# Kernel tuning notes

Hardware: AMD Instinct MI355X
Metric: run time of the kernel (lower is better)

## Reference

```python
import jax, jax.numpy as jnp
import numpy as np
from jax import lax

N = 2_097_152  # grid length
WENO5_MULT_BIAS = 0.1


def _conv1d(x, w, b, pad):
    # x: [1, C_in, L], w: [C_out, C_in, K] -> [1, C_out, L]
    y = lax.conv_general_dilated(x, w, window_strides=(1,), padding=[(pad, pad)],
                                 dimension_numbers=('NCH', 'OIH', 'NCH'))
    return y + b[None, :, None]


def _inner_nn_weno5(dif, w1, b1, w2, b2, w3, b3, w4, b4, w5, b5, w6, b6):
    # dif: [N] -> multiplier signal [N] in (0,1) via sigmoid
    x = dif[None, None, :]
    x = jax.nn.elu(_conv1d(x, w1, b1, 2))
    x = jax.nn.elu(_conv1d(x, w2, b2, 2))
    x = jax.nn.elu(_conv1d(x, w3, b3, 0))
    x = jax.nn.elu(_conv1d(x, w4, b4, 0))
    x = jax.nn.elu(_conv1d(x, w5, b5, 1))
    x = jax.nn.sigmoid(_conv1d(x, w6, b6, 0))
    return x[0, 0, :]


def _avg_diff(uu):
    # centered average of forward differences, replicated at the edges -> [N]
    dif = uu[1:] - uu[:-1]
    dif_left = jnp.concatenate([dif, dif[-1:]])
    dif_right = jnp.concatenate([dif[:1], dif])
    return 0.5 * dif_left + 0.5 * dif_right


def _fluxes_minus(u):
    f0 = (11 * u[3:-2] - 7 * u[4:-1] + 2 * u[5:]) / 6
    f1 = (2 * u[2:-3] + 5 * u[3:-2] - u[4:-1]) / 6
    f2 = (-u[1:-4] + 5 * u[2:-3] + 2 * u[3:-2]) / 6
    return f0, f1, f2


def _betas_minus(u):
    b0 = 13 / 12 * (u[3:-2] - 2 * u[4:-1] + u[5:]) ** 2 + 1 / 4 * (3 * u[3:-2] - 4 * u[4:-1] + u[5:]) ** 2
    b1 = 13 / 12 * (u[2:-3] - 2 * u[3:-2] + u[4:-1]) ** 2 + 1 / 4 * (u[2:-3] - u[4:-1]) ** 2
    b2 = 13 / 12 * (u[1:-4] - 2 * u[2:-3] + u[3:-2]) ** 2 + 1 / 4 * (u[1:-4] - 4 * u[2:-3] + 3 * u[3:-2]) ** 2
    return b0, b1, b2


def _weno5(uu, e, beta_mult):
    # w5_minus=True, mweno=True, mapped=False, trainable=True branch
    ur = uu[1:]
    ul = uu[:-1]
    fp = _fluxes_minus(ur)
    fn = _fluxes_minus(ul)
    bp = _betas_minus(ur)
    bn = _betas_minus(ul)
    # multipliers bm[3+shift:-3+shift] for shift in {-1,0,1}
    mul = (beta_mult[2:-4], beta_mult[3:-3], beta_mult[4:-2])
    bp = [b * m for b, m in zip(bp, mul)]
    bn = [b * m for b, m in zip(bn, mul)]
    ds = (1 / 10, 6 / 10, 3 / 10)

    def omegas_mweno(bs):
        brs = (bs[2] - bs[0]) ** 2
        o = [d / (e + b) ** 2 * (brs + (e + b) ** 2) for b, d in zip(bs, ds)]
        s = o[0] + o[1] + o[2]
        return [x / s for x in o]

    op = omegas_mweno(bp)
    on = omegas_mweno(bn)
    fluxp = op[0] * fp[0] + op[1] * fp[1] + op[2] * fp[2]
    fluxn = on[0] * fn[0] + on[1] * fn[1] + on[2] * fn[2]
    return fluxp - fluxn  # [N-6]


def setup_inputs() -> dict:
    key = jax.random.key(0)
    ks = jax.random.split(key, 14)
    uu = jax.random.normal(ks[0], (N,), dtype=jnp.float32)
    e = jnp.float32(1e-6)
    s = 0.1  # weight scale for stability
    w1 = s * jax.random.normal(ks[1], (20, 1, 5), jnp.float32)
    b1 = s * jax.random.normal(ks[2], (20,), jnp.float32)
    w2 = s * jax.random.normal(ks[3], (40, 20, 5), jnp.float32)
    b2 = s * jax.random.normal(ks[4], (40,), jnp.float32)
    w3 = s * jax.random.normal(ks[5], (80, 40, 1), jnp.float32)
    b3 = s * jax.random.normal(ks[6], (80,), jnp.float32)
    w4 = s * jax.random.normal(ks[7], (40, 80, 1), jnp.float32)
    b4 = s * jax.random.normal(ks[8], (40,), jnp.float32)
    w5 = s * jax.random.normal(ks[9], (20, 40, 3), jnp.float32)
    b5 = s * jax.random.normal(ks[10], (20,), jnp.float32)
    w6 = s * jax.random.normal(ks[11], (1, 20, 1), jnp.float32)
    b6 = s * jax.random.normal(ks[12], (1,), jnp.float32)
    return {"uu": uu, "e": e, "w1": w1, "b1": b1, "w2": w2, "b2": b2,
            "w3": w3, "b3": b3, "w4": w4, "b4": b4, "w5": w5, "b5": b5,
            "w6": w6, "b6": b6}


def reference(uu, e, w1, b1, w2, b2, w3, b3, w4, b4, w5, b5, w6, b6):
    dif = _avg_diff(uu)
    beta_mult = _inner_nn_weno5(dif, w1, b1, w2, b2, w3, b3, w4, b4, w5, b5, w6, b6) + WENO5_MULT_BIAS
    return _weno5(uu, e, beta_mult)
```

## Files before the change

### kernel.cpp

```cpp
#include <hip/hip_runtime.h>
#include <math.h>

#define NTHREADS 256
#define TOUT 126
#define NP 128
#define X1S 40
#define T3S 88
#define X5S 26
#define NDIF 136
#define NDIFP 152
#define NUU 138
#define WREG 2816

#define F2_BASE 0
#define F3_BASE 15
#define F4_BASE 25
#define F5_BASE 34
#define F1_BASE 42
#define NFRAGS 44

typedef unsigned short u16;
typedef unsigned int u32;
typedef __attribute__((ext_vector_type(8))) short bf16x8;
typedef __attribute__((ext_vector_type(4))) float f32x4;

__device__ __forceinline__ float elu_f(float x) {
    return fmaxf(x, __expf(fminf(x, 0.0f)) - 1.0f);
}
__device__ __forceinline__ float rcp_f(float x) {
    return __builtin_amdgcn_rcpf(x);
}
__device__ __forceinline__ float sq_f(float x) { return x * x; }
__device__ __forceinline__ u16 f2bf(float f) {
    union { float f; u32 u; } v; v.f = f;
    u32 r = v.u + 0x7FFFu + ((v.u >> 16) & 1u);
    return (u16)(r >> 16);
}
__device__ __forceinline__ float bf2f(u16 h) {
    union { u32 u; float f; } v; v.u = ((u32)h) << 16;
    return v.f;
}
__device__ __forceinline__ u32 pack_trunc(float a, float b) {
    union { float f; u32 u; } va, vb; va.f = a; vb.f = b;
#if __has_builtin(__builtin_amdgcn_perm)
    return __builtin_amdgcn_perm(vb.u, va.u, 0x07060302u);
#else
    return (vb.u & 0xFFFF0000u) | (va.u >> 16);
#endif
}
__device__ __forceinline__ u32 pack_rne(float a, float b) {
    return (u32)f2bf(a) | ((u32)f2bf(b) << 16);
}

__global__ __launch_bounds__(64) void build_frags_kernel(
    const float* __restrict__ w1, const float* __restrict__ w2,
    const float* __restrict__ w3, const float* __restrict__ w4,
    const float* __restrict__ w5, u16* __restrict__ ws)
{
    const int f = blockIdx.x;
    const int lane = threadIdx.x;
    const int m = lane & 15;
    const int q = lane >> 4;
    float wvv[8];
    #pragma unroll
    for (int j = 0; j < 8; ++j) wvv[j] = 0.0f;

    if (f < F3_BASE) {
        int mt = (f - F2_BASE) / 5, s = (f - F2_BASE) % 5;
        int oc = mt * 16 + m;
        #pragma unroll
        for (int j = 0; j < 8; ++j) {
            int ic = q * 8 + j;
            if (oc < 40 && ic < 20) wvv[j] = w2[oc * 100 + ic * 5 + s];
        }
    } else if (f < F4_BASE) {
        int mt = (f - F3_BASE) / 2, s = (f - F3_BASE) % 2;
        int oc = mt * 16 + m;
        #pragma unroll
        for (int j = 0; j < 8; ++j) {
            int k = s * 32 + q * 8 + j;
            if (k < 40) wvv[j] = w3[oc * 40 + k];
        }
    } else if (f < F5_BASE) {
        int mt = (f - F4_BASE) / 3, s = (f - F4_BASE) % 3;
        int oc = mt * 16 + m;
        #pragma unroll
        for (int j = 0; j < 8; ++j) {
            int k = s * 32 + q * 8 + j;
            if (oc < 40 && k < 80) wvv[j] = w4[oc * 80 + k];
        }
    } else if (f < F1_BASE) {
        int mt = (f - F5_BASE) / 4, s = (f - F5_BASE) % 4;
        int oc = mt * 16 + m;
        int k0 = s * 32 + q * 8;
        int dk = k0 / 40, ic0 = k0 - dk * 40;
        #pragma unroll
        for (int j = 0; j < 8; ++j) {
            if (oc < 20 && k0 < 120) wvv[j] = w5[oc * 120 + (ic0 + j) * 3 + dk];
        }
    } else {
        int mt = f - F1_BASE;
        int oc = mt * 16 + m;
        #pragma unroll
        for (int j = 0; j < 8; ++j) {
            int k = q * 8 + j;
            if (oc < 20 && k < 5) wvv[j] = w1[oc * 5 + k];
        }
    }
    u32 pk[4];
    #pragma unroll
    for (int p = 0; p < 4; ++p)
        pk[p] = (u32)f2bf(wvv[2 * p]) | ((u32)f2bf(wvv[2 * p + 1]) << 16);
    u32* wp = (u32*)&ws[(f * 64 + lane) * 8];
    wp[0] = pk[0]; wp[1] = pk[1]; wp[2] = pk[2]; wp[3] = pk[3];
}

__device__ __forceinline__ bf16x8 ld_frag(const u16* ws, int f, int lane) {
    return *(const bf16x8*)&ws[(f * 64 + lane) * 8];
}

__global__ __launch_bounds__(NTHREADS, 2) void weno_nn_kernel(
    const float* __restrict__ uu, const float* __restrict__ e_ptr,
    const float* __restrict__ w1, const float* __restrict__ b1,
    const float* __restrict__ b2, const float* __restrict__ b3,
    const float* __restrict__ b4, const float* __restrict__ b5,
    const float* __restrict__ w6, const float* __restrict__ b6,
    const u16* __restrict__ wfr,
    float* __restrict__ out, int n_out, int N)
{
    __shared__ float s_uu[NUU];
    __shared__ float s_dif[NDIFP];
    __shared__ __align__(16) u16 bufA[4 * WREG];
    __shared__ __align__(16) u16 bufB[130 * 40];

    float* s_beta = s_dif;

    const int tid  = threadIdx.x;
    const int lane = tid & 63;
    const int wv_id = __builtin_amdgcn_readfirstlane(tid >> 6);
    const int m    = lane & 15;
    const int q    = lane >> 4;
    const int J0   = blockIdx.x * TOUT;
    const int P0   = J0 + 2;
    const int U0   = J0 - 4;

    u16* xw = &bufA[wv_id * WREG];

    for (int i = tid; i < NUU; i += NTHREADS) {
        int g = U0 + i;
        s_uu[i] = (g >= 0 && g < N) ? uu[g] : 0.0f;
    }
    __syncthreads();

    for (int d = tid; d < NDIFP; d += NTHREADS) {
        int g = P0 - 5 + d;
        float v = 0.0f;
        if (d < NDIF && g >= 0 && g < N) {
            int j1 = g < N - 2 ? g : N - 2;
            int j0 = g - 1 > 0 ? g - 1 : 0;
            float dl = s_uu[j1 + 1 - U0] - s_uu[j1 - U0];
            float dr = s_uu[j0 + 1 - U0] - s_uu[j0 - U0];
            v = 0.5f * (dl + dr);
        }
        s_dif[d] = v;
    }
    __syncthreads();


    {
        bf16x8 a1[2];
        a1[0] = ld_frag(wfr, F1_BASE + 0, lane);
        a1[1] = ld_frag(wfr, F1_BASE + 1, lane);
        f32x4 bias1[2];
        #pragma unroll
        for (int r = 0; r < 4; ++r) {
            bias1[0][r] = b1[4 * q + r];
            int oc = 16 + 4 * q + r;
            bias1[1][r] = (oc < 20) ? b1[oc] : 0.0f;
        }
        #pragma unroll
        for (int it = 0; it < 3; ++it) {
            const int li = it * 16 + m;
            const int pos = wv_id * 32 + li;
            float d0 = s_dif[pos + 0];
            float d1 = s_dif[pos + 1];
            float d2 = s_dif[pos + 2];
            float d3 = s_dif[pos + 3];
            float d4 = s_dif[pos + 4];
            bf16x8 bfrag;
            u32* bw = (u32*)&bfrag;
            bw[0] = pack_rne(d0, d1);
            bw[1] = pack_rne(d2, d3);
            bw[2] = pack_rne(d4, 0.0f);
            bw[3] = 0;
            f32x4 acc0 = bias1[0];
            f32x4 acc1 = bias1[1];
            acc0 = __builtin_amdgcn_mfma_f32_16x16x32_bf16(a1[0], bfrag, acc0, 0, 0, 0);
            acc1 = __builtin_amdgcn_mfma_f32_16x16x32_bf16(a1[1], bfrag, acc1, 0, 0, 0);
            if (li < 36) {
                int g = P0 - 3 + pos;
                bool valid = (g >= 0 && g < N);
                float e0 = valid ? elu_f(acc0[0]) : 0.0f;
                float e1 = valid ? elu_f(acc0[1]) : 0.0f;
                float e2 = valid ? elu_f(acc0[2]) : 0.0f;
                float e3 = valid ? elu_f(acc0[3]) : 0.0f;
                u32* wp = (u32*)&xw[li * X1S + 4 * q];
                wp[0] = pack_trunc(e0, e1);
                wp[1] = pack_trunc(e2, e3);
                if (q == 0) {
                    float f0 = valid ? elu_f(acc1[0]) : 0.0f;
                    float f1 = valid ? elu_f(acc1[1]) : 0.0f;
                    float f2 = valid ? elu_f(acc1[2]) : 0.0f;
                    float f3 = valid ? elu_f(acc1[3]) : 0.0f;
                    u32* wp2 = (u32*)&xw[li * X1S + 16];
                    wp2[0] = pack_trunc(f0, f1);
                    wp2[1] = pack_trunc(f2, f3);
                } else {
                    u32* wpz = (u32*)&xw[li * X1S + 20 + (q - 1) * 4];
                    wpz[0] = 0; wpz[1] = 0;
                }
            }
        }
    }
    __builtin_amdgcn_sched_barrier(0);

    {
        bf16x8 a2[3][5];
        #pragma unroll
        for (int mt = 0; mt < 3; ++mt)
            #pragma unroll
            for (int s = 0; s < 5; ++s)
                a2[mt][s] = ld_frag(wfr, F2_BASE + mt * 5 + s, lane);
        f32x4 bias2[3];
        #pragma unroll
        for (int mt = 0; mt < 3; ++mt) {
            #pragma unroll
            for (int r = 0; r < 4; ++r) {
                int oc = mt * 16 + 4 * q + r;
                bias2[mt][r] = (oc < 40) ? b2[oc] : 0.0f;
            }
        }
        for (int t = 0; t < 2; ++t) {
            const int lr = t * 16 + m;
            const int gr = wv_id * 32 + lr;
            f32x4 acc[3];
            #pragma unroll
            for (int mt = 0; mt < 3; ++mt) acc[mt] = bias2[mt];
            #pragma unroll
            for (int s = 0; s < 5; ++s) {
                bf16x8 bfrag = *(const bf16x8*)&xw[(lr + s) * X1S + q * 8];
                #pragma unroll
                for (int mt = 0; mt < 3; ++mt)
                    acc[mt] = __builtin_amdgcn_mfma_f32_16x16x32_bf16(a2[mt][s], bfrag, acc[mt], 0, 0, 0);
            }
            #pragma unroll
            for (int mt = 0; mt < 3; ++mt) {
                int oc0 = mt * 16 + 4 * q;
                if (oc0 < 40) {
                    u32* wp = (u32*)&bufB[gr * 40 + oc0];
                    wp[0] = pack_trunc(elu_f(acc[mt][0]), elu_f(acc[mt][1]));
                    wp[1] = pack_trunc(elu_f(acc[mt][2]), elu_f(acc[mt][3]));
                }
            }
        }
    }
    __builtin_amdgcn_sched_barrier(0);

    {
        bf16x8 a3[5][2];
        #pragma unroll
        for (int mt = 0; mt < 5; ++mt)
            #pragma unroll
            for (int s = 0; s < 2; ++s)
                a3[mt][s] = ld_frag(wfr, F3_BASE + mt * 2 + s, lane);
        f32x4 bias3[5];
        #pragma unroll
        for (int mt = 0; mt < 5; ++mt) {
            #pragma unroll
            for (int r = 0; r < 4; ++r) bias3[mt][r] = b3[mt * 16 + 4 * q + r];
        }
        for (int t = 0; t < 2; ++t) {
            const int lr = t * 16 + m;
            const int gr = wv_id * 32 + lr;
            f32x4 acc[5];
            #pragma unroll
            for (int mt = 0; mt < 5; ++mt) acc[mt] = bias3[mt];
            {
                bf16x8 bfrag = *(const bf16x8*)&bufB[gr * 40 + q * 8];
                #pragma unroll
                for (int mt = 0; mt < 5; ++mt)
                    acc[mt] = __builtin_amdgcn_mfma_f32_16x16x32_bf16(a3[mt][0], bfrag, acc[mt], 0, 0, 0);
            }
            {
                bf16x8 bfrag = *(const bf16x8*)&bufB[gr * 40 + ((q == 0) ? 32 : 0)];
                #pragma unroll
                for (int mt = 0; mt < 5; ++mt)
                    acc[mt] = __builtin_amdgcn_mfma_f32_16x16x32_bf16(a3[mt][1], bfrag, acc[mt], 0, 0, 0);
            }
            #pragma unroll
            for (int mt = 0; mt < 5; ++mt) {
                int oc0 = mt * 16 + 4 * q;
                u32* wp = (u32*)&xw[lr * T3S + oc0];
                wp[0] = pack_trunc(elu_f(acc[mt][0]), elu_f(acc[mt][1]));
                wp[1] = pack_trunc(elu_f(acc[mt][2]), elu_f(acc[mt][3]));
            }
        }
    }
    __builtin_amdgcn_sched_barrier(0);

    {
        bf16x8 a4[3][3];
        #pragma unroll
        for (int mt = 0; mt < 3; ++mt)
            #pragma unroll
            for (int s = 0; s < 3; ++s)
                a4[mt][s] = ld_frag(wfr, F4_BASE + mt * 3 + s, lane);
        f32x4 bias4[3];
        #pragma unroll
        for (int mt = 0; mt < 3; ++mt) {
            #pragma unroll
            for (int r = 0; r < 4; ++r) {
                int oc = mt * 16 + 4 * q + r;
                bias4[mt][r] = (oc < 40) ? b4[oc] : 0.0f;
            }
        }
        if (tid < 80) bufB[128 * 40 + tid] = 0;
        for (int t = 0; t < 2; ++t) {
            const int lr = t * 16 + m;
            const int gr = wv_id * 32 + lr;
            f32x4 acc[3];
            #pragma unroll
            for (int mt = 0; mt < 3; ++mt) acc[mt] = bias4[mt];
            #pragma unroll
            for (int s = 0; s < 3; ++s) {
                int k0 = s * 32 + q * 8;
                bf16x8 bfrag = *(const bf16x8*)&xw[lr * T3S + ((k0 < 80) ? k0 : 0)];
                #pragma unroll
                for (int mt = 0; mt < 3; ++mt)
                    acc[mt] = __builtin_amdgcn_mfma_f32_16x16x32_bf16(a4[mt][s], bfrag, acc[mt], 0, 0, 0);
            }
            #pragma unroll
            for (int mt = 0; mt < 3; ++mt) {
                int oc0 = mt * 16 + 4 * q;
                if (oc0 < 40) {
                    u32* wp = (u32*)&bufB[gr * 40 + oc0];
                    wp[0] = pack_trunc(elu_f(acc[mt][0]), elu_f(acc[mt][1]));
                    wp[1] = pack_trunc(elu_f(acc[mt][2]), elu_f(acc[mt][3]));
                }
            }
        }
    }
    __syncthreads();

    {
        bf16x8 a5[2][4];
        #pragma unroll
        for (int mt = 0; mt < 2; ++mt)
            #pragma unroll
            for (int s = 0; s < 4; ++s)
                a5[mt][s] = ld_frag(wfr, F5_BASE + mt * 4 + s, lane);
        f32x4 bias5[2];
        #pragma unroll
        for (int mt = 0; mt < 2; ++mt) {
            #pragma unroll
            for (int r = 0; r < 4; ++r) {
                int oc = mt * 16 + 4 * q + r;
                bias5[mt][r] = (oc < 20) ? b5[oc] : 0.0f;
            }
        }
        for (int t = 0; t < 2; ++t) {
            const int N0 = (wv_id * 2 + t) * 16;
            f32x4 acc[2];
            #pragma unroll
            for (int mt = 0; mt < 2; ++mt) acc[mt] = bias5[mt];
            #pragma unroll
            for (int s = 0; s < 4; ++s) {
                int k0 = s * 32 + q * 8;
                int dk = (k0 < 120) ? (k0 / 40) : 0;
                int ic0 = (k0 < 120) ? (k0 - dk * 40) : 0;
                bf16x8 bfrag = *(const bf16x8*)&bufB[(N0 + m + dk) * 40 + ic0];
                #pragma unroll
                for (int mt = 0; mt < 2; ++mt)
                    acc[mt] = __builtin_amdgcn_mfma_f32_16x16x32_bf16(a5[mt][s], bfrag, acc[mt], 0, 0, 0);
            }
            #pragma unroll
            for (int mt = 0; mt < 2; ++mt) {
                int oc0 = mt * 16 + 4 * q;
                if (oc0 < 20) {
                    u32* wp = (u32*)&bufA[(N0 + m) * X5S + oc0];
                    wp[0] = pack_trunc(elu_f(acc[mt][0]), elu_f(acc[mt][1]));
                    wp[1] = pack_trunc(elu_f(acc[mt][2]), elu_f(acc[mt][3]));
                }
            }
        }
    }
    __syncthreads();

    if (tid < NP) {
        float a = b6[0];
        #pragma unroll
        for (int c = 0; c < 20; ++c)
            a += w6[c] * bf2f(bufA[tid * X5S + c]);
        s_beta[tid] = rcp_f(1.0f + __expf(-a)) + 0.1f;
    }
    __syncthreads();

    const float eps = e_ptr[0];
    if (tid < TOUT) {
        int j = J0 + tid;
        if (j < n_out) {
            float a  = s_uu[tid + 5];
            float b  = s_uu[tid + 6];
            float c  = s_uu[tid + 7];
            float d  = s_uu[tid + 8];
            float ee = s_uu[tid + 9];
            float f  = s_uu[tid + 10];
            float m0 = s_beta[tid];
            float m1 = s_beta[tid + 1];
            float m2 = s_beta[tid + 2];

            const float i6 = 1.0f / 6.0f;
            float fp0 = (11.f * d - 7.f * ee + 2.f * f) * i6;
            float fp1 = (2.f * c + 5.f * d - ee) * i6;
            float fp2 = (-b + 5.f * c + 2.f * d) * i6;
            float fn0 = (11.f * c - 7.f * d + 2.f * ee) * i6;
            float fn1 = (2.f * b + 5.f * c - d) * i6;
            float fn2 = (-a + 5.f * b + 2.f * c) * i6;

            const float c1312 = 13.f / 12.f;
            float bp0 = c1312 * sq_f(d - 2.f * ee + f) + 0.25f * sq_f(3.f * d - 4.f * ee + f);
            float bp1 = c1312 * sq_f(c - 2.f * d + ee) + 0.25f * sq_f(c - ee);
            float bp2 = c1312 * sq_f(b - 2.f * c + d) + 0.25f * sq_f(b - 4.f * c + 3.f * d);
            float bn0 = c1312 * sq_f(c - 2.f * d + ee) + 0.25f * sq_f(3.f * c - 4.f * d + ee);
            float bn1 = c1312 * sq_f(b - 2.f * c + d) + 0.25f * sq_f(b - d);
            float bn2 = c1312 * sq_f(a - 2.f * b + c) + 0.25f * sq_f(a - 4.f * b + 3.f * c);

            bp0 *= m0; bp1 *= m1; bp2 *= m2;
            bn0 *= m0; bn1 *= m1; bn2 *= m2;

            float q0 = eps + bp0; q0 *= q0;
            float q1 = eps + bp1; q1 *= q1;
            float q2 = eps + bp2; q2 *= q2;
            float brs = bp2 - bp0; brs *= brs;
            float o0 = 0.1f * (1.f + brs * rcp_f(q0));
            float o1 = 0.6f * (1.f + brs * rcp_f(q1));
            float o2 = 0.3f * (1.f + brs * rcp_f(q2));
            float inv = rcp_f(o0 + o1 + o2);
            float fluxp = (o0 * fp0 + o1 * fp1 + o2 * fp2) * inv;

            q0 = eps + bn0; q0 *= q0;
            q1 = eps + bn1; q1 *= q1;
            q2 = eps + bn2; q2 *= q2;
            brs = bn2 - bn0; brs *= brs;
            o0 = 0.1f * (1.f + brs * rcp_f(q0));
            o1 = 0.6f * (1.f + brs * rcp_f(q1));
            o2 = 0.3f * (1.f + brs * rcp_f(q2));
            inv = rcp_f(o0 + o1 + o2);
            float fluxn = (o0 * fn0 + o1 * fn1 + o2 * fn2) * inv;

            out[j] = fluxp - fluxn;
        }
    }
}

extern "C" void kernel_launch(void* const* d_in, const int* in_sizes, int n_in,
                              void* d_out, int out_size, void* d_ws, size_t ws_size,
                              hipStream_t stream) {
    const float* uu = (const float*)d_in[0];
    const float* e  = (const float*)d_in[1];
    const float* w1 = (const float*)d_in[2];
    const float* b1 = (const float*)d_in[3];
    const float* w2 = (const float*)d_in[4];
    const float* b2 = (const float*)d_in[5];
    const float* w3 = (const float*)d_in[6];
    const float* b3 = (const float*)d_in[7];
    const float* w4 = (const float*)d_in[8];
    const float* b4 = (const float*)d_in[9];
    const float* w5 = (const float*)d_in[10];
    const float* b5 = (const float*)d_in[11];
    const float* w6 = (const float*)d_in[12];
    const float* b6 = (const float*)d_in[13];
    float* out = (float*)d_out;
    u16* wfr = (u16*)d_ws;
    const int N = in_sizes[0];
    const int nblocks = (out_size + TOUT - 1) / TOUT;

    build_frags_kernel<<<NFRAGS, 64, 0, stream>>>(w1, w2, w3, w4, w5, wfr);
    weno_nn_kernel<<<nblocks, NTHREADS, 0, stream>>>(
        uu, e, w1, b1, b2, b3, b4, b5, w6, b6, wfr,
        out, out_size, N);
}
```

Measured before the change: 257.9 us.

## Fold log2e into weights, fuse final conv+sigmoid into layer 5, shrink tile rows

Pre-scales the conv weights and biases by log2(e) so each ELU becomes a bare exp2 plus an fma, with the final 1x1 conv weights rescaled by ln2 to compensate. The final 1x1 conv and sigmoid are fused into the layer-5 epilogue using cross-lane shuffles, which removes a shared-memory round trip and one block barrier. The difference signal is stored as packed bf16 pairs so layer 1 builds its fragments with three loads instead of five loads and packs. Per-wave rows drop from 32 to 30 (118 outputs per block), so less halo is recomputed in waste lanes, but more blocks are launched and the halo work is a larger share of each block.

```diff
diff --git a/kernel.cpp b/kernel.cpp
--- a/kernel.cpp
+++ b/kernel.cpp
@@ -2,15 +2,17 @@
 #include <math.h>
 
 #define NTHREADS 256
-#define TOUT 126
-#define NP 128
+#define TOUT 118
+#define NP 120
+#define WROWS 30
 #define X1S 40
 #define T3S 88
-#define X5S 26
-#define NDIF 136
-#define NDIFP 152
-#define NUU 138
-#define WREG 2816
+#define NDIF 128
+#define NDIFP 144
+#define NUU 130
+#define WREG (WROWS * T3S)
+#define LOG2E 1.44269504f
+#define LN2   0.69314718f
 
 #define F2_BASE 0
 #define F3_BASE 15
@@ -24,8 +26,16 @@
 typedef __attribute__((ext_vector_type(8))) short bf16x8;
 typedef __attribute__((ext_vector_type(4))) float f32x4;
 
-__device__ __forceinline__ float elu_f(float x) {
-    return fmaxf(x, __expf(fminf(x, 0.0f)) - 1.0f);
+__device__ __forceinline__ float exp2_f(float x) {
+#if __has_builtin(__builtin_amdgcn_exp2f)
+    return __builtin_amdgcn_exp2f(x);
+#else
+    float r; asm("v_exp_f32 %0, %1" : "=v"(r) : "v"(x)); return r;
+#endif
+}
+__device__ __forceinline__ float eluc_f(float y) {
+    float t = exp2_f(fminf(y, 0.0f));
+    return fmaxf(y, fmaf(t, LOG2E, -LOG2E));
 }
 __device__ __forceinline__ float rcp_f(float x) {
     return __builtin_amdgcn_rcpf(x);
@@ -35,10 +45,6 @@
     union { float f; u32 u; } v; v.f = f;
     u32 r = v.u + 0x7FFFu + ((v.u >> 16) & 1u);
     return (u16)(r >> 16);
-}
-__device__ __forceinline__ float bf2f(u16 h) {
-    union { u32 u; float f; } v; v.u = ((u32)h) << 16;
-    return v.f;
 }
 __device__ __forceinline__ u32 pack_trunc(float a, float b) {
     union { float f; u32 u; } va, vb; va.f = a; vb.f = b;
@@ -104,7 +110,7 @@
         #pragma unroll
         for (int j = 0; j < 8; ++j) {
             int k = q * 8 + j;
-            if (oc < 20 && k < 5) wvv[j] = w1[oc * 5 + k];
+            if (oc < 20 && k < 5) wvv[j] = w1[oc * 5 + k] * LOG2E;
         }
     }
     u32 pk[4];
@@ -129,11 +135,11 @@
     float* __restrict__ out, int n_out, int N)
 {
     __shared__ float s_uu[NUU];
-    __shared__ float s_dif[NDIFP];
+    __shared__ u32 s_difh[NDIFP];
     __shared__ __align__(16) u16 bufA[4 * WREG];
-    __shared__ __align__(16) u16 bufB[130 * 40];
-
-    float* s_beta = s_dif;
+    __shared__ __align__(16) u16 bufB[(NP + 2) * 40];
+
+    float* s_beta = (float*)s_difh;
 
     const int tid  = threadIdx.x;
     const int lane = tid & 63;
@@ -152,17 +158,19 @@
     }
     __syncthreads();
 
-    for (int d = tid; d < NDIFP; d += NTHREADS) {
-        int g = P0 - 5 + d;
-        float v = 0.0f;
-        if (d < NDIF && g >= 0 && g < N) {
+    {
+        auto difval = [&](int d) -> float {
+            if (d >= NDIF) return 0.0f;
+            int g = P0 - 5 + d;
+            if (g < 0 || g >= N) return 0.0f;
             int j1 = g < N - 2 ? g : N - 2;
             int j0 = g - 1 > 0 ? g - 1 : 0;
             float dl = s_uu[j1 + 1 - U0] - s_uu[j1 - U0];
             float dr = s_uu[j0 + 1 - U0] - s_uu[j0 - U0];
-            v = 0.5f * (dl + dr);
-        }
-        s_dif[d] = v;
+            return 0.5f * (dl + dr);
+        };
+        for (int d = tid; d < NDIFP; d += NTHREADS)
+            s_difh[d] = pack_rne(difval(d), difval(d + 1));
     }
     __syncthreads();
 
@@ -174,44 +182,39 @@
         f32x4 bias1[2];
         #pragma unroll
         for (int r = 0; r < 4; ++r) {
-            bias1[0][r] = b1[4 * q + r];
+            bias1[0][r] = b1[4 * q + r] * LOG2E;
             int oc = 16 + 4 * q + r;
-            bias1[1][r] = (oc < 20) ? b1[oc] : 0.0f;
+            bias1[1][r] = (oc < 20) ? b1[oc] * LOG2E : 0.0f;
         }
         #pragma unroll
         for (int it = 0; it < 3; ++it) {
             const int li = it * 16 + m;
-            const int pos = wv_id * 32 + li;
-            float d0 = s_dif[pos + 0];
-            float d1 = s_dif[pos + 1];
-            float d2 = s_dif[pos + 2];
-            float d3 = s_dif[pos + 3];
-            float d4 = s_dif[pos + 4];
+            const int pos = wv_id * WROWS + li;
             bf16x8 bfrag;
             u32* bw = (u32*)&bfrag;
-            bw[0] = pack_rne(d0, d1);
-            bw[1] = pack_rne(d2, d3);
-            bw[2] = pack_rne(d4, 0.0f);
+            bw[0] = s_difh[pos];
+            bw[1] = s_difh[pos + 2];
+            bw[2] = s_difh[pos + 4];
             bw[3] = 0;
             f32x4 acc0 = bias1[0];
             f32x4 acc1 = bias1[1];
             acc0 = __builtin_amdgcn_mfma_f32_16x16x32_bf16(a1[0], bfrag, acc0, 0, 0, 0);
             acc1 = __builtin_amdgcn_mfma_f32_16x16x32_bf16(a1[1], bfrag, acc1, 0, 0, 0);
-            if (li < 36) {
+            if (li < WROWS + 4) {
                 int g = P0 - 3 + pos;
                 bool valid = (g >= 0 && g < N);
-                float e0 = valid ? elu_f(acc0[0]) : 0.0f;
-                float e1 = valid ? elu_f(acc0[1]) : 0.0f;
-                float e2 = valid ? elu_f(acc0[2]) : 0.0f;
-                float e3 = valid ? elu_f(acc0[3]) : 0.0f;
+                float e0 = valid ? eluc_f(acc0[0]) : 0.0f;
+                float e1 = valid ? eluc_f(acc0[1]) : 0.0f;
+                float e2 = valid ? eluc_f(acc0[2]) : 0.0f;
+                float e3 = valid ? eluc_f(acc0[3]) : 0.0f;
                 u32* wp = (u32*)&xw[li * X1S + 4 * q];
                 wp[0] = pack_trunc(e0, e1);
                 wp[1] = pack_trunc(e2, e3);
                 if (q == 0) {
-                    float f0 = valid ? elu_f(acc1[0]) : 0.0f;
-                    float f1 = valid ? elu_f(acc1[1]) : 0.0f;
-                    float f2 = valid ? elu_f(acc1[2]) : 0.0f;
-                    float f3 = valid ? elu_f(acc1[3]) : 0.0f;
+                    float f0 = valid ? eluc_f(acc1[0]) : 0.0f;
+                    float f1 = valid ? eluc_f(acc1[1]) : 0.0f;
+                    float f2 = valid ? eluc_f(acc1[2]) : 0.0f;
+                    float f3 = valid ? eluc_f(acc1[3]) : 0.0f;
                     u32* wp2 = (u32*)&xw[li * X1S + 16];
                     wp2[0] = pack_trunc(f0, f1);
                     wp2[1] = pack_trunc(f2, f3);
@@ -237,12 +240,12 @@
             #pragma unroll
             for (int r = 0; r < 4; ++r) {
                 int oc = mt * 16 + 4 * q + r;
-                bias2[mt][r] = (oc < 40) ? b2[oc] : 0.0f;
+                bias2[mt][r] = (oc < 40) ? b2[oc] * LOG2E : 0.0f;
             }
         }
         for (int t = 0; t < 2; ++t) {
             const int lr = t * 16 + m;
-            const int gr = wv_id * 32 + lr;
+            const int gr = wv_id * WROWS + lr;
             f32x4 acc[3];
             #pragma unroll
             for (int mt = 0; mt < 3; ++mt) acc[mt] = bias2[mt];
@@ -256,10 +259,10 @@
             #pragma unroll
             for (int mt = 0; mt < 3; ++mt) {
                 int oc0 = mt * 16 + 4 * q;
-                if (oc0 < 40) {
+                if (lr < WROWS && oc0 < 40) {
                     u32* wp = (u32*)&bufB[gr * 40 + oc0];
-                    wp[0] = pack_trunc(elu_f(acc[mt][0]), elu_f(acc[mt][1]));
-                    wp[1] = pack_trunc(elu_f(acc[mt][2]), elu_f(acc[mt][3]));
+                    wp[0] = pack_trunc(eluc_f(acc[mt][0]), eluc_f(acc[mt][1]));
+                    wp[1] = pack_trunc(eluc_f(acc[mt][2]), eluc_f(acc[mt][3]));
                 }
             }
         }
@@ -277,11 +280,11 @@
         #pragma unroll
         for (int mt = 0; mt < 5; ++mt) {
             #pragma unroll
-            for (int r = 0; r < 4; ++r) bias3[mt][r] = b3[mt * 16 + 4 * q + r];
+            for (int r = 0; r < 4; ++r) bias3[mt][r] = b3[mt * 16 + 4 * q + r] * LOG2E;
         }
         for (int t = 0; t < 2; ++t) {
             const int lr = t * 16 + m;
-            const int gr = wv_id * 32 + lr;
+            const int gr = wv_id * WROWS + lr;
             f32x4 acc[5];
             #pragma unroll
             for (int mt = 0; mt < 5; ++mt) acc[mt] = bias3[mt];
@@ -300,9 +303,11 @@
             #pragma unroll
             for (int mt = 0; mt < 5; ++mt) {
                 int oc0 = mt * 16 + 4 * q;
-                u32* wp = (u32*)&xw[lr * T3S + oc0];
-                wp[0] = pack_trunc(elu_f(acc[mt][0]), elu_f(acc[mt][1]));
-                wp[1] = pack_trunc(elu_f(acc[mt][2]), elu_f(acc[mt][3]));
+                if (lr < WROWS) {
+                    u32* wp = (u32*)&xw[lr * T3S + oc0];
+                    wp[0] = pack_trunc(eluc_f(acc[mt][0]), eluc_f(acc[mt][1]));
+                    wp[1] = pack_trunc(eluc_f(acc[mt][2]), eluc_f(acc[mt][3]));
+                }
             }
         }
     }
@@ -321,13 +326,13 @@
             #pragma unroll
             for (int r = 0; r < 4; ++r) {
                 int oc = mt * 16 + 4 * q + r;
-                bias4[mt][r] = (oc < 40) ? b4[oc] : 0.0f;
-            }
-        }
-        if (tid < 80) bufB[128 * 40 + tid] = 0;
+                bias4[mt][r] = (oc < 40) ? b4[oc] * LOG2E : 0.0f;
+            }
+        }
+        if (tid < 80) bufB[NP * 40 + tid] = 0;
         for (int t = 0; t < 2; ++t) {
             const int lr = t * 16 + m;
-            const int gr = wv_id * 32 + lr;
+            const int gr = wv_id * WROWS + lr;
             f32x4 acc[3];
             #pragma unroll
             for (int mt = 0; mt < 3; ++mt) acc[mt] = bias4[mt];
@@ -342,10 +347,10 @@
             #pragma unroll
             for (int mt = 0; mt < 3; ++mt) {
                 int oc0 = mt * 16 + 4 * q;
-                if (oc0 < 40) {
+                if (lr < WROWS && oc0 < 40) {
                     u32* wp = (u32*)&bufB[gr * 40 + oc0];
-                    wp[0] = pack_trunc(elu_f(acc[mt][0]), elu_f(acc[mt][1]));
-                    wp[1] = pack_trunc(elu_f(acc[mt][2]), elu_f(acc[mt][3]));
+                    wp[0] = pack_trunc(eluc_f(acc[mt][0]), eluc_f(acc[mt][1]));
+                    wp[1] = pack_trunc(eluc_f(acc[mt][2]), eluc_f(acc[mt][3]));
                 }
             }
         }
@@ -365,11 +370,20 @@
             #pragma unroll
             for (int r = 0; r < 4; ++r) {
                 int oc = mt * 16 + 4 * q + r;
-                bias5[mt][r] = (oc < 20) ? b5[oc] : 0.0f;
-            }
-        }
+                bias5[mt][r] = (oc < 20) ? b5[oc] * LOG2E : 0.0f;
+            }
+        }
+        float w6a[4], w6b[4];
+        #pragma unroll
+        for (int r = 0; r < 4; ++r) {
+            w6a[r] = w6[4 * q + r] * LN2;
+            w6b[r] = (q == 0) ? w6[16 + r] * LN2 : 0.0f;
+        }
+        const float b6v = b6[0];
+
         for (int t = 0; t < 2; ++t) {
             const int N0 = (wv_id * 2 + t) * 16;
+            const int row = N0 + m;
             f32x4 acc[2];
             #pragma unroll
             for (int mt = 0; mt < 2; ++mt) acc[mt] = bias5[mt];
@@ -378,30 +392,24 @@
                 int k0 = s * 32 + q * 8;
                 int dk = (k0 < 120) ? (k0 / 40) : 0;
                 int ic0 = (k0 < 120) ? (k0 - dk * 40) : 0;
-                bf16x8 bfrag = *(const bf16x8*)&bufB[(N0 + m + dk) * 40 + ic0];
+                int rr = row + dk;
+                rr = (rr < NP + 2) ? rr : (NP + 1);
+                bf16x8 bfrag = *(const bf16x8*)&bufB[rr * 40 + ic0];
                 #pragma unroll
                 for (int mt = 0; mt < 2; ++mt)
                     acc[mt] = __builtin_amdgcn_mfma_f32_16x16x32_bf16(a5[mt][s], bfrag, acc[mt], 0, 0, 0);
             }
-            #pragma unroll
-            for (int mt = 0; mt < 2; ++mt) {
-                int oc0 = mt * 16 + 4 * q;
-                if (oc0 < 20) {
-                    u32* wp = (u32*)&bufA[(N0 + m) * X5S + oc0];
-                    wp[0] = pack_trunc(elu_f(acc[mt][0]), elu_f(acc[mt][1]));
-                    wp[1] = pack_trunc(elu_f(acc[mt][2]), elu_f(acc[mt][3]));
-                }
-            }
-        }
-    }
-    __syncthreads();
-
-    if (tid < NP) {
-        float a = b6[0];
-        #pragma unroll
-        for (int c = 0; c < 20; ++c)
-            a += w6[c] * bf2f(bufA[tid * X5S + c]);
-        s_beta[tid] = rcp_f(1.0f + __expf(-a)) + 0.1f;
+            float p = 0.0f;
+            #pragma unroll
+            for (int r = 0; r < 4; ++r) p += w6a[r] * eluc_f(acc[0][r]);
+            #pragma unroll
+            for (int r = 0; r < 4; ++r) p += w6b[r] * eluc_f(acc[1][r]);
+            p += __shfl_xor(p, 16);
+            p += __shfl_xor(p, 32);
+            float aa = p + b6v;
+            if (q == 0 && row < NP)
+                s_beta[row] = rcp_f(1.0f + __expf(-aa)) + 0.1f;
+        }
     }
     __syncthreads();
 
```

Measured after the change: 295.5 us. 1.15x slower.
